# Performance work log

Measured on AMD Instinct MI355X. Metric: run time of the kernel, lower is better.

The kernel has to match this reference:

```python
import jax, jax.numpy as jnp
import numpy as np

SOS_TOKEN = 2
T = 1024      # sequence / max_length
H = 256       # embedding_dim == GRU hidden size
V = 50000     # vocab_size


def gru_cell(e, h, w_ih, w_hh, b_ih, b_hh):
    # PyTorch nn.GRU cell math. e, h: [H]; w_ih, w_hh: [3H, H]; b_*: [3H]
    gi = w_ih @ e + b_ih
    gh = w_hh @ h + b_hh
    i_r, i_z, i_n = jnp.split(gi, 3)
    h_r, h_z, h_n = jnp.split(gh, 3)
    r = jax.nn.sigmoid(i_r + h_r)
    z = jax.nn.sigmoid(i_z + h_z)
    n = jnp.tanh(i_n + r * h_n)
    return (1.0 - z) * n + z * h


def setup_inputs() -> dict:
    key = jax.random.key(0)
    ks = jax.random.split(key, 14)
    s = 1.0 / np.sqrt(H)
    def u(k, shape):
        return jax.random.uniform(k, shape, jnp.float32, -s, s)
    return {
        "x": jax.random.randint(ks[0], (T,), 0, V),
        "enc_emb": jax.random.normal(ks[1], (V, H), jnp.float32),
        "enc_w_ih": u(ks[2], (3 * H, H)),
        "enc_w_hh": u(ks[3], (3 * H, H)),
        "enc_b_ih": u(ks[4], (3 * H,)),
        "enc_b_hh": u(ks[5], (3 * H,)),
        "dec_emb": jax.random.normal(ks[6], (V, H), jnp.float32),
        "dec_w_ih": u(ks[7], (3 * H, H)),
        "dec_w_hh": u(ks[8], (3 * H, H)),
        "dec_b_ih": u(ks[9], (3 * H,)),
        "dec_b_hh": u(ks[10], (3 * H,)),
        "w_out": u(ks[11], (V, H)),
        "b_out": u(ks[12], (V,)),
    }


def reference(x, enc_emb, enc_w_ih, enc_w_hh, enc_b_ih, enc_b_hh,
              dec_emb, dec_w_ih, dec_w_hh, dec_b_ih, dec_b_hh, w_out, b_out):
    # ---- Encoder: embed whole sequence, scan GRU to final hidden ----
    emb_seq = enc_emb[x]                      # [T, H] (no relu in encoder)

    def enc_step(h, e):
        return gru_cell(e, h, enc_w_ih, enc_w_hh, enc_b_ih, enc_b_hh), None

    h_enc, _ = jax.lax.scan(enc_step, jnp.zeros((H,), emb_seq.dtype), emb_seq)

    # ---- Decoder: greedy argmax feedback, per-step log-softmax ----
    def dec_step(carry, _):
        h, tok = carry
        e = jax.nn.relu(dec_emb[tok])         # embed + relu
        h = gru_cell(e, h, dec_w_ih, dec_w_hh, dec_b_ih, dec_b_hh)
        logits = w_out @ h + b_out            # [V]
        logp = jax.nn.log_softmax(logits)
        tok = jnp.argmax(logp)                # topk(1) greedy feedback
        return (h, tok), logp

    init = (h_enc, jnp.asarray(SOS_TOKEN, x.dtype))
    _, decoder_outputs = jax.lax.scan(dec_step, init, None, length=T)
    return decoder_outputs                    # [T, V] log-probs
```

## Files before the change

### kernel.cpp

```cpp
#include <hip/hip_runtime.h>
#include <stdint.h>

#define TSEQ 1024
#define H 256
#define H3 768
#define NV 50000
#define NBLK 256
#define NTHR 512
#define RPB 196
#define SOS_TOK 2
#define SPIN_LIM (1 << 20)
#define NEB 4
#define EEL 64
#define EROWS 192

#define WS_SALT   0
#define WS_HENC   1024
#define WS_PMX    8192
#define WS_REC    16384
#define WS_GIENC  65536
#define WS_TABLE  (65536 + TSEQ * H3 * 4)
#define TABLE_BYTES ((size_t)NV * H3 * 4)

using u64 = unsigned long long;

__device__ __forceinline__ void awr(u64* p, u64 v) {
  __hip_atomic_store(p, v, __ATOMIC_RELAXED, __HIP_MEMORY_SCOPE_AGENT);
}
__device__ __forceinline__ u64 ard(u64* p) {
  return __hip_atomic_load(p, __ATOMIC_RELAXED, __HIP_MEMORY_SCOPE_AGENT);
}
__device__ __forceinline__ u64 pkf(unsigned tg, float f) {
  return ((u64)tg << 32) | (u64)__float_as_uint(f);
}
__device__ __forceinline__ float upf(u64 w) { return __uint_as_float((unsigned)w); }
__device__ __forceinline__ unsigned tagof(u64 w) { return (unsigned)(w >> 32); }

__device__ __forceinline__ void agpr_w(float& dst, float v) {
  asm volatile("v_accvgpr_write_b32 %0, %1" : "=a"(dst) : "v"(v));
}
__device__ __forceinline__ float agpr_r(float src) {
  float v;
  asm volatile("v_accvgpr_read_b32 %0, %1" : "=v"(v) : "a"(src));
  return v;
}

extern "C" __global__ void k_init(char* ws) {
  if (threadIdx.x == 0) {
    unsigned* s = (unsigned*)(ws + WS_SALT);
    *s = *s + 1u;
  }
}

extern "C" __global__ void k_enc_gi(const int* __restrict__ x, const float* __restrict__ emb,
                                    const float* __restrict__ wih, const float* __restrict__ bih,
                                    float* __restrict__ gi) {
  int tid = threadIdx.x;
  int t0 = blockIdx.x * 16;
  __shared__ float4 se4[16][H / 4];
  float* se = (float*)se4;
  for (int idx = tid; idx < 16 * H; idx += 256) {
    int j = idx >> 8, k = idx & 255;
    se[j * H + k] = emb[(size_t)x[t0 + j] * H + k];
  }
  __syncthreads();
  for (int q = 0; q < 3; q++) {
    int r = q * H + tid;
    const float4* w4 = (const float4*)(wih + (size_t)r * H);
    float bb = bih[r];
    float a[16];
#pragma unroll
    for (int j = 0; j < 16; j++) a[j] = bb;
    for (int k = 0; k < H / 4; k++) {
      float4 wv = w4[k];
#pragma unroll
      for (int j = 0; j < 16; j++) {
        float4 ev = se4[j][k];
        a[j] += wv.x * ev.x + wv.y * ev.y + wv.z * ev.z + wv.w * ev.w;
      }
    }
#pragma unroll
    for (int j = 0; j < 16; j++) gi[(size_t)(t0 + j) * H3 + r] = a[j];
  }
}

extern "C" __global__ void k_table(const float* __restrict__ emb, const float* __restrict__ wih,
                                   const float* __restrict__ bih, float* __restrict__ table) {
  int tid = threadIdx.x;
  int v0 = blockIdx.x * 16;
  __shared__ float4 se4[16][H / 4];
  float* se = (float*)se4;
  for (int idx = tid; idx < 16 * H; idx += 256) {
    int j = idx >> 8, k = idx & 255;
    se[j * H + k] = fmaxf(emb[(size_t)(v0 + j) * H + k], 0.f);
  }
  __syncthreads();
  for (int q = 0; q < 3; q++) {
    int r = q * H + tid;
    const float4* w4 = (const float4*)(wih + (size_t)r * H);
    float bb = bih[r];
    float a[16];
#pragma unroll
    for (int j = 0; j < 16; j++) a[j] = bb;
    for (int k = 0; k < H / 4; k++) {
      float4 wv = w4[k];
#pragma unroll
      for (int j = 0; j < 16; j++) {
        float4 ev = se4[j][k];
        a[j] += wv.x * ev.x + wv.y * ev.y + wv.z * ev.z + wv.w * ev.w;
      }
    }
#pragma unroll
    for (int j = 0; j < 16; j++) table[(size_t)(v0 + j) * H3 + r] = a[j];
  }
}

extern "C" __global__ void __launch_bounds__(NTHR, 1)
k_enc(const float* __restrict__ enc_whh, const float* __restrict__ enc_bhh,
      char* __restrict__ ws) {
  const int b = blockIdx.x, tid = threadIdx.x;
  u64* henc = (u64*)(ws + WS_HENC);
  const float* gi_enc = (const float*)(ws + WS_GIENC);
  __shared__ float sh_h[H];
  __shared__ float sh_ghE[EROWS];
  __shared__ int sh_abort;
  if (tid == 0) sh_abort = 0;

  const int p2 = tid >> 1, hf = tid & 1;
  const bool ract = (p2 < EROWS);
  const int q = p2 >> 6, ri = p2 & 63;
  const size_t grow = ract ? (size_t)(q * H + b * EEL + ri) : 0;
  float wa[128];
  {
    const float4* wp = (const float4*)(enc_whh + grow * H + hf * 128);
#pragma unroll
    for (int k = 0; k < 32; ++k) {
      float4 v = ract ? wp[k] : make_float4(0.f, 0.f, 0.f, 0.f);
      agpr_w(wa[4 * k + 0], v.x);
      agpr_w(wa[4 * k + 1], v.y);
      agpr_w(wa[4 * k + 2], v.z);
      agpr_w(wa[4 * k + 3], v.w);
    }
  }
  const int el = b * EEL + tid;
  float be0 = 0.f, be1 = 0.f, be2 = 0.f;
  if (tid < EEL) { be0 = enc_bhh[el]; be1 = enc_bhh[H + el]; be2 = enc_bhh[2 * H + el]; }
  const unsigned salt = *(volatile unsigned*)(ws + WS_SALT);
  const unsigned tb32 = salt * 65536u;
  __syncthreads();

  float hb = 0.f;
  if (tid < EEL) {
    float g0 = gi_enc[el], g1 = gi_enc[H + el], g2 = gi_enc[2 * H + el];
    float r = 1.f / (1.f + expf(-(g0 + be0)));
    float z = 1.f / (1.f + expf(-(g1 + be1)));
    float n = tanhf(g2 + r * be2);
    hb = (1.f - z) * n;
    awr(henc + 256 + el, pkf(tb32 + 1u, hb));
  }
  int ec = 1;
  for (int t = 1; t < TSEQ; ++t) {
    float g0 = 0.f, g1 = 0.f, g2 = 0.f;
    if (tid < EEL) {
      g0 = gi_enc[(size_t)t * H3 + el];
      g1 = gi_enc[(size_t)t * H3 + H + el];
      g2 = gi_enc[(size_t)t * H3 + 2 * H + el];
    }
    if (tid < H) {
      u64* pp_ = henc + (size_t)(ec & 1) * 256 + tid;
      u64 w = 0; int n_ = 0;
      do { w = ard(pp_); } while (tagof(w) != tb32 + (unsigned)ec && ++n_ < SPIN_LIM);
      if (tagof(w) != tb32 + (unsigned)ec) sh_abort = 1;
      sh_h[tid] = upf(w);
    }
    __syncthreads();
    if (sh_abort) return;
    float pcc = 0.f;
    if (ract) {
      const float4* h4 = ((const float4*)sh_h) + hf * 32;
#pragma unroll
      for (int k = 0; k < 32; ++k) {
        float4 hv = h4[k];
        pcc += agpr_r(wa[4 * k + 0]) * hv.x + agpr_r(wa[4 * k + 1]) * hv.y +
               agpr_r(wa[4 * k + 2]) * hv.z + agpr_r(wa[4 * k + 3]) * hv.w;
      }
    }
    pcc += __shfl_xor(pcc, 1);
    if (ract && hf == 0) sh_ghE[p2] = pcc;
    __syncthreads();
    ++ec;
    if (tid < EEL) {
      float r = 1.f / (1.f + expf(-(g0 + (sh_ghE[tid] + be0))));
      float z = 1.f / (1.f + expf(-(g1 + (sh_ghE[EEL + tid] + be1))));
      float n = tanhf(g2 + r * (sh_ghE[2 * EEL + tid] + be2));
      hb = (1.f - z) * n + z * hb;
      awr(henc + (size_t)(ec & 1) * 256 + el, pkf(tb32 + (unsigned)ec, hb));
    }
  }
}

extern "C" __global__ void __launch_bounds__(NTHR, 1)
k_dec(const float* __restrict__ dec_emb, const float* __restrict__ dec_wih,
      const float* __restrict__ dec_whh, const float* __restrict__ dec_bih,
      const float* __restrict__ dec_bhh, const float* __restrict__ w_out,
      const float* __restrict__ b_out, float* __restrict__ out,
      char* __restrict__ ws, int use_table) {
  const int b = blockIdx.x, tid = threadIdx.x;
  u64* henc = (u64*)(ws + WS_HENC);
  u64* pmx = (u64*)(ws + WS_PMX);
  u64* rec = (u64*)(ws + WS_REC);
  const float* table = (const float*)(ws + WS_TABLE);

  __shared__ float sh_h[H];
  __shared__ float sh_wd[3][H];
  __shared__ float sh_wi[3][H];
  __shared__ float sh_gi[H3];
  __shared__ float gh_lds[H3];
  __shared__ float sh_lg[2][RPB];
  __shared__ float sh_bout[RPB];
  __shared__ float sh_gh3[3];
  __shared__ float sh_rv[8];
  __shared__ float sh_mv[8];
  __shared__ int sh_mi[8];
  __shared__ float sh_sv[8];
  __shared__ float sh_mv2[8];
  __shared__ int sh_mi2[8];
  __shared__ float sh_sv2[8];
  __shared__ float sh_e[H];
  __shared__ int sh_abort;

  if (tid == 0) sh_abort = 0;

  for (int k = tid; k < 3 * H; k += NTHR) {
    int q = k >> 8, c = k & 255;
    sh_wd[q][c] = dec_whh[((size_t)(3 * b + q)) * H + c];
    if (!use_table) sh_wi[q][c] = dec_wih[((size_t)(3 * b + q)) * H + c];
  }
  const float bd0 = dec_bhh[3 * b], bd1 = dec_bhh[3 * b + 1], bd2 = dec_bhh[3 * b + 2];
  float bi0 = 0.f, bi1 = 0.f, bi2 = 0.f;
  if (!use_table) { bi0 = dec_bih[3 * b]; bi1 = dec_bih[3 * b + 1]; bi2 = dec_bih[3 * b + 2]; }
  const int rowbase = b * RPB;
  const int nrows = min(RPB, max(0, NV - rowbase));
  const int p = tid >> 1, hf = tid & 1;
  const bool wact = (p < nrows);
  float wa[128];
  {
    const float4* wp = (const float4*)(w_out + (size_t)(rowbase + (wact ? p : 0)) * H + hf * 128);
#pragma unroll
    for (int i = 0; i < 32; ++i) {
      float4 v = wact ? wp[i] : make_float4(0.f, 0.f, 0.f, 0.f);
      agpr_w(wa[4 * i + 0], v.x);
      agpr_w(wa[4 * i + 1], v.y);
      agpr_w(wa[4 * i + 2], v.z);
      agpr_w(wa[4 * i + 3], v.w);
    }
  }
  if (tid < RPB) sh_bout[tid] = (tid < nrows) ? b_out[rowbase + tid] : 0.f;
  const unsigned salt = *(volatile unsigned*)(ws + WS_SALT);
  const unsigned tb32 = salt * 65536u;
  const unsigned tb24 = salt * 4096u;
  __syncthreads();

  auto wave_maxidx = [&](float& mv, int& mi) {
#pragma unroll
    for (int off = 32; off >= 1; off >>= 1) {
      float ov = __shfl_xor(mv, off);
      int oi = __shfl_xor(mi, off);
      if (ov > mv || (ov == mv && oi < mi)) { mv = ov; mi = oi; }
    }
  };
  auto row3 = [&](const float(&wr)[3][H], float bb0, float bb1, float bb2, const float* vin) {
    int q = tid >> 7, i = tid & 127;
    float pp = 0.f;
    if (q < 3) pp = wr[q][2 * i] * vin[2 * i] + wr[q][2 * i + 1] * vin[2 * i + 1];
#pragma unroll
    for (int off = 32; off >= 1; off >>= 1) pp += __shfl_xor(pp, off);
    if (q < 3 && (tid & 63) == 0) sh_rv[tid >> 6] = pp;
    __syncthreads();
    if (tid == 0) {
      sh_gh3[0] = sh_rv[0] + sh_rv[1] + bb0;
      sh_gh3[1] = sh_rv[2] + sh_rv[3] + bb1;
      sh_gh3[2] = sh_rv[4] + sh_rv[5] + bb2;
    }
    __syncthreads();
  };
  auto gru_step = [&]() {
    if (tid < H) {
      float gir = sh_gi[tid], giz = sh_gi[H + tid], gin = sh_gi[2 * H + tid];
      float ghr = gh_lds[tid], ghz = gh_lds[H + tid], ghn = gh_lds[2 * H + tid];
      float r = 1.f / (1.f + expf(-(gir + ghr)));
      float z = 1.f / (1.f + expf(-(giz + ghz)));
      float n = tanhf(gin + r * ghn);
      sh_h[tid] = (1.f - z) * n + z * sh_h[tid];
    }
    __syncthreads();
  };
  auto spin_rec3 = [&](unsigned tg, float* dst) {
    if (tid < NBLK) {
      u64* pp_ = rec + (size_t)(tg & 1) * 1024 + (size_t)tid * 4;
      u64 w0 = 0, w1 = 0, w2 = 0; int n = 0; bool ok;
      do {
        w0 = ard(pp_ + 0); w1 = ard(pp_ + 1); w2 = ard(pp_ + 2);
        ok = (tagof(w0) == tg) & (tagof(w1) == tg) & (tagof(w2) == tg);
      } while (!ok && ++n < SPIN_LIM);
      if (!ok) sh_abort = 1;
      dst[3 * tid] = upf(w0); dst[3 * tid + 1] = upf(w1); dst[3 * tid + 2] = upf(w2);
    }
    __syncthreads();
  };

  if (tid < NBLK) {
    u64* pp_ = henc + tid;
    u64 w = 0; int n_ = 0;
    do { w = ard(pp_); } while (tagof(w) != tb32 + (unsigned)TSEQ && ++n_ < SPIN_LIM);
    if (tagof(w) != tb32 + (unsigned)TSEQ) sh_abort = 1;
    sh_h[tid] = upf(w);
  }
  __syncthreads();
  if (sh_abort) return;

  int e = TSEQ;
  row3(sh_wd, bd0, bd1, bd2, sh_h);
  ++e;
  {
    unsigned tg = tb32 + (unsigned)e;
    if (tid == 0) {
      u64* d = rec + (size_t)(tg & 1) * 1024 + (size_t)b * 4;
      awr(d + 0, pkf(tg, sh_gh3[0]));
      awr(d + 1, pkf(tg, sh_gh3[1]));
      awr(d + 2, pkf(tg, sh_gh3[2]));
    }
    spin_rec3(tg, gh_lds);
    if (sh_abort) return;
  }

  int tok = SOS_TOK;
  float2 gp = make_float2(0.f, 0.f);
  if (use_table) {
    if (tid < 384) gp = *(const float2*)(table + (size_t)SOS_TOK * H3 + 2 * tid);
  } else {
    for (int j = tid; j < H; j += NTHR) sh_e[j] = fmaxf(dec_emb[(size_t)SOS_TOK * H + j], 0.f);
    __syncthreads();
    row3(sh_wi, bi0, bi1, bi2, sh_e);
    ++e;
    unsigned tg = tb32 + (unsigned)e;
    if (tid == 0) {
      u64* d = rec + (size_t)(tg & 1) * 1024 + (size_t)b * 4;
      awr(d + 0, pkf(tg, sh_gh3[0]));
      awr(d + 1, pkf(tg, sh_gh3[1]));
      awr(d + 2, pkf(tg, sh_gh3[2]));
    }
    spin_rec3(tg, sh_gi);
    if (sh_abort) return;
  }

  float lse_pend = 0.f;
  for (int t = 0; t < TSEQ; ++t) {
    const int cur = t & 1;
    if (use_table) {
      if (tid < 384) { sh_gi[2 * tid] = gp.x; sh_gi[2 * tid + 1] = gp.y; }
    }
    __syncthreads();
    gru_step();
    float acc = 0.f;
    if (wact) {
      const float4* h4 = ((const float4*)sh_h) + hf * 32;
#pragma unroll
      for (int i = 0; i < 32; ++i) {
        float4 hv = h4[i];
        acc += agpr_r(wa[4 * i + 0]) * hv.x + agpr_r(wa[4 * i + 1]) * hv.y +
               agpr_r(wa[4 * i + 2]) * hv.z + agpr_r(wa[4 * i + 3]) * hv.w;
      }
    }
    acc += __shfl_xor(acc, 1);
    if (wact && hf == 0) sh_lg[cur][p] = acc + sh_bout[p];
    __syncthreads();
    ++e;
    const unsigned tg32 = tb32 + (unsigned)e;
    const unsigned tg24 = (tb24 + (unsigned)e) & 0xFFFFFFu;
    float mv = (tid < nrows) ? sh_lg[cur][tid] : -INFINITY;
    int mi = (tid < nrows) ? (rowbase + tid) : 0x7fffffff;
    wave_maxidx(mv, mi);
    if ((tid & 63) == 0) { sh_mv[tid >> 6] = mv; sh_mi[tid >> 6] = mi; }
    __syncthreads();
    float bmax = sh_mv[0]; int bidx = sh_mi[0];
#pragma unroll
    for (int k = 1; k < 8; ++k)
      if (sh_mv[k] > bmax || (sh_mv[k] == bmax && sh_mi[k] < bidx)) { bmax = sh_mv[k]; bidx = sh_mi[k]; }
    if (tid == 0) {
      u64 g = ((u64)tg24 << 40) | ((u64)__float_as_uint(bmax) << 8) |
              (u64)((unsigned)(bidx - rowbase) & 0xFFu);
      awr(pmx + (size_t)(e & 1) * 256 + b, g);
    }
    float ec = (tid < nrows) ? __expf(sh_lg[cur][tid] - bmax) : 0.f;
#pragma unroll
    for (int off = 32; off >= 1; off >>= 1) ec += __shfl_xor(ec, off);
    if ((tid & 63) == 0) sh_sv[tid >> 6] = ec;
    __syncthreads();
    float bsum = 0.f;
#pragma unroll
    for (int k = 0; k < 8; ++k) bsum += sh_sv[k];
    row3(sh_wd, bd0, bd1, bd2, sh_h);
    if (tid == 0) {
      u64* d = rec + (size_t)(e & 1) * 1024 + (size_t)b * 4;
      awr(d + 0, pkf(tg32, sh_gh3[0]));
      awr(d + 1, pkf(tg32, sh_gh3[1]));
      awr(d + 2, pkf(tg32, sh_gh3[2]));
      awr(d + 3, pkf(tg32, bsum));
    }
    if (t > 0 && tid < nrows)
      out[(size_t)(t - 1) * NV + rowbase + tid] = sh_lg[cur ^ 1][tid] - lse_pend;
    float bm_e = -INFINITY; int ie = 0x7fffffff;
    {
      u64 w = 0;
      if (tid < NBLK) {
        u64* pp_ = pmx + (size_t)(e & 1) * 256 + tid;
        int n = 0;
        do { w = ard(pp_); } while ((unsigned)(w >> 40) != tg24 && ++n < SPIN_LIM);
        if ((unsigned)(w >> 40) != tg24) sh_abort = 1;
        bm_e = __uint_as_float((unsigned)((w >> 8) & 0xFFFFFFFFu));
        ie = tid * RPB + (int)(w & 0xFFu);
      }
      __syncthreads();
      if (sh_abort) return;
    }
    float mv2 = bm_e; int mi2 = ie;
    wave_maxidx(mv2, mi2);
    if ((tid & 63) == 0) { sh_mv2[tid >> 6] = mv2; sh_mi2[tid >> 6] = mi2; }
    __syncthreads();
    float gmax = sh_mv2[0]; int gidx = sh_mi2[0];
#pragma unroll
    for (int k = 1; k < 8; ++k)
      if (sh_mv2[k] > gmax || (sh_mv2[k] == gmax && sh_mi2[k] < gidx)) { gmax = sh_mv2[k]; gidx = sh_mi2[k]; }
    tok = gidx;
    if (use_table && t + 1 < TSEQ) {
      if (tid < 384) gp = *(const float2*)(table + (size_t)tok * H3 + 2 * tid);
    }
    float sv = 0.f;
    if (tid < NBLK) {
      u64* pp_ = rec + (size_t)(e & 1) * 1024 + (size_t)tid * 4;
      u64 w0 = 0, w1 = 0, w2 = 0, w3 = 0; int n = 0; bool ok;
      do {
        w0 = ard(pp_ + 0); w1 = ard(pp_ + 1); w2 = ard(pp_ + 2); w3 = ard(pp_ + 3);
        ok = (tagof(w0) == tg32) & (tagof(w1) == tg32) & (tagof(w2) == tg32) &
             (tagof(w3) == tg32);
      } while (!ok && ++n < SPIN_LIM);
      if (!ok) sh_abort = 1;
      gh_lds[3 * tid] = upf(w0); gh_lds[3 * tid + 1] = upf(w1); gh_lds[3 * tid + 2] = upf(w2);
      sv = upf(w3);
    }
    __syncthreads();
    if (sh_abort) return;
    float c = (tid < NBLK) ? sv * __expf(bm_e - gmax) : 0.f;
#pragma unroll
    for (int off = 32; off >= 1; off >>= 1) c += __shfl_xor(c, off);
    if ((tid & 63) == 0) sh_sv2[tid >> 6] = c;
    __syncthreads();
    float S = 0.f;
#pragma unroll
    for (int k = 0; k < 8; ++k) S += sh_sv2[k];
    lse_pend = gmax + logf(S);
    if (!use_table && t + 1 < TSEQ) {
      for (int j = tid; j < H; j += NTHR) sh_e[j] = fmaxf(dec_emb[(size_t)tok * H + j], 0.f);
      __syncthreads();
      row3(sh_wi, bi0, bi1, bi2, sh_e);
      ++e;
      unsigned tgg = tb32 + (unsigned)e;
      if (tid == 0) {
        u64* d = rec + (size_t)(tgg & 1) * 1024 + (size_t)b * 4;
        awr(d + 0, pkf(tgg, sh_gh3[0]));
        awr(d + 1, pkf(tgg, sh_gh3[1]));
        awr(d + 2, pkf(tgg, sh_gh3[2]));
      }
      spin_rec3(tgg, sh_gi);
      if (sh_abort) return;
    }
  }
  if (tid < nrows)
    out[(size_t)(TSEQ - 1) * NV + rowbase + tid] = sh_lg[(TSEQ - 1) & 1][tid] - lse_pend;
}

extern "C" void kernel_launch(void* const* d_in, const int* in_sizes, int n_in,
                              void* d_out, int out_size, void* d_ws, size_t ws_size,
                              hipStream_t stream) {
  (void)in_sizes; (void)n_in; (void)out_size;
  const int* x = (const int*)d_in[0];
  const float* enc_emb = (const float*)d_in[1];
  const float* enc_wih = (const float*)d_in[2];
  const float* enc_whh = (const float*)d_in[3];
  const float* enc_bih = (const float*)d_in[4];
  const float* enc_bhh = (const float*)d_in[5];
  const float* dec_emb = (const float*)d_in[6];
  const float* dec_wih = (const float*)d_in[7];
  const float* dec_whh = (const float*)d_in[8];
  const float* dec_bih = (const float*)d_in[9];
  const float* dec_bhh = (const float*)d_in[10];
  const float* w_out = (const float*)d_in[11];
  const float* b_out = (const float*)d_in[12];
  float* out = (float*)d_out;
  char* ws = (char*)d_ws;

  int use_table = (ws_size >= (size_t)WS_TABLE + TABLE_BYTES) ? 1 : 0;

  k_init<<<1, 64, 0, stream>>>(ws);
  k_enc_gi<<<TSEQ / 16, 256, 0, stream>>>(x, enc_emb, enc_wih, enc_bih, (float*)(ws + WS_GIENC));
  if (use_table)
    k_table<<<NV / 16, 256, 0, stream>>>(dec_emb, dec_wih, dec_bih, (float*)(ws + WS_TABLE));
  k_enc<<<NEB, NTHR, 0, stream>>>(enc_whh, enc_bhh, ws);
  k_dec<<<NBLK, NTHR, 0, stream>>>(dec_emb, dec_wih, dec_whh, dec_bih, dec_bhh,
                                   w_out, b_out, out, ws, use_table);
}
```

Baseline: 9.354 ms.

## Overlap decoder table build with encoder scan and colocate encoder blocks on one XCD

The separate table kernel is folded into the encoder launch. 64 blocks start, and four of them, chosen through an XCD-ID roster so they share one XCD, run the serial encoder GRU. The rest pull table tiles from a dynamic atomic counter, so the table precompute overlaps the latency-bound encoder scan. When all four workers are on the same XCD and a probe handshake succeeds, they exchange hidden state through workgroup-scope stores and L2 atomic reads instead of agent-scope traffic, with a fallback to the old path otherwise. The decoder also defers the log-sum-exp reduction by one step, so it runs after the partial-sum publish rather than in the critical exchange path. This adds spin-based roster and verdict handshakes, and relies on the XCD placement and L2-coherence assumptions holding.

Measured after the change: 8.644 ms. -7.6%, faster.

```diff
diff --git a/kernel.cpp b/kernel.cpp
--- a/kernel.cpp
+++ b/kernel.cpp
@@ -10,14 +10,19 @@
 #define RPB 196
 #define SOS_TOK 2
 #define SPIN_LIM (1 << 20)
-#define NEB 4
+#define NEB_L 64
+#define NEW 4
 #define EEL 64
 #define EROWS 192
 
 #define WS_SALT   0
+#define WS_DISP   64
+#define WS_ROSTER 128
+#define WS_VERD   832
 #define WS_HENC   1024
 #define WS_PMX    8192
 #define WS_REC    16384
+#define WS_EHL2   32768
 #define WS_GIENC  65536
 #define WS_TABLE  (65536 + TSEQ * H3 * 4)
 #define TABLE_BYTES ((size_t)NV * H3 * 4)
@@ -30,11 +35,27 @@
 __device__ __forceinline__ u64 ard(u64* p) {
   return __hip_atomic_load(p, __ATOMIC_RELAXED, __HIP_MEMORY_SCOPE_AGENT);
 }
+__device__ __forceinline__ unsigned ard32(unsigned* p) {
+  return __hip_atomic_load(p, __ATOMIC_RELAXED, __HIP_MEMORY_SCOPE_AGENT);
+}
 __device__ __forceinline__ u64 pkf(unsigned tg, float f) {
   return ((u64)tg << 32) | (u64)__float_as_uint(f);
 }
+__device__ __forceinline__ u64 pku(unsigned tg, unsigned v) {
+  return ((u64)tg << 32) | (u64)v;
+}
 __device__ __forceinline__ float upf(u64 w) { return __uint_as_float((unsigned)w); }
 __device__ __forceinline__ unsigned tagof(u64 w) { return (unsigned)(w >> 32); }
+
+__device__ __forceinline__ void wgst(u64* p, u64 v) {
+  __hip_atomic_store(p, v, __ATOMIC_RELAXED, __HIP_MEMORY_SCOPE_WORKGROUP);
+}
+__device__ __forceinline__ u64 wgld(u64* p) {
+  u64 v;
+  asm volatile("global_atomic_add_x2 %0, %1, %2, off sc0\n\ts_waitcnt vmcnt(0)"
+               : "=v"(v) : "v"(p), "v"(0ull) : "memory");
+  return v;
+}
 
 __device__ __forceinline__ void agpr_w(float& dst, float v) {
   asm volatile("v_accvgpr_write_b32 %0, %1" : "=a"(dst) : "v"(v));
@@ -49,6 +70,8 @@
   if (threadIdx.x == 0) {
     unsigned* s = (unsigned*)(ws + WS_SALT);
     *s = *s + 1u;
+    *(unsigned*)(ws + WS_DISP) = 0u;
+    for (int i = 0; i < 8; ++i) *(unsigned*)(ws + WS_ROSTER + i * 64) = 0u;
   }
 }
 
@@ -84,52 +107,124 @@
   }
 }
 
-extern "C" __global__ void k_table(const float* __restrict__ emb, const float* __restrict__ wih,
-                                   const float* __restrict__ bih, float* __restrict__ table) {
-  int tid = threadIdx.x;
-  int v0 = blockIdx.x * 16;
-  __shared__ float4 se4[16][H / 4];
-  float* se = (float*)se4;
-  for (int idx = tid; idx < 16 * H; idx += 256) {
-    int j = idx >> 8, k = idx & 255;
-    se[j * H + k] = fmaxf(emb[(size_t)(v0 + j) * H + k], 0.f);
-  }
-  __syncthreads();
-  for (int q = 0; q < 3; q++) {
-    int r = q * H + tid;
-    const float4* w4 = (const float4*)(wih + (size_t)r * H);
-    float bb = bih[r];
-    float a[16];
-#pragma unroll
-    for (int j = 0; j < 16; j++) a[j] = bb;
-    for (int k = 0; k < H / 4; k++) {
-      float4 wv = w4[k];
-#pragma unroll
-      for (int j = 0; j < 16; j++) {
-        float4 ev = se4[j][k];
-        a[j] += wv.x * ev.x + wv.y * ev.y + wv.z * ev.z + wv.w * ev.w;
-      }
-    }
-#pragma unroll
-    for (int j = 0; j < 16; j++) table[(size_t)(v0 + j) * H3 + r] = a[j];
-  }
-}
-
 extern "C" __global__ void __launch_bounds__(NTHR, 1)
 k_enc(const float* __restrict__ enc_whh, const float* __restrict__ enc_bhh,
-      char* __restrict__ ws) {
+      const float* __restrict__ dec_emb, const float* __restrict__ dec_wih,
+      const float* __restrict__ dec_bih, char* __restrict__ ws, int use_table) {
   const int b = blockIdx.x, tid = threadIdx.x;
   u64* henc = (u64*)(ws + WS_HENC);
+  u64* ehl2 = (u64*)(ws + WS_EHL2);
+  u64* verd = (u64*)(ws + WS_VERD);
   const float* gi_enc = (const float*)(ws + WS_GIENC);
+  float* table = (float*)(ws + WS_TABLE);
+
+  __shared__ float se[16 * H];
   __shared__ float sh_h[H];
   __shared__ float sh_ghE[EROWS];
-  __shared__ int sh_abort;
+  __shared__ int sh_xcd, sh_rank, sh_chosen, sh_u, sh_abort;
   if (tid == 0) sh_abort = 0;
+
+  const unsigned salt = *(volatile unsigned*)(ws + WS_SALT);
+  const unsigned tb32 = salt * 65536u;
+
+  if (tid == 0) {
+    unsigned x;
+    asm volatile("s_getreg_b32 %0, hwreg(HW_REG_XCC_ID)" : "=s"(x));
+    int myxcd = (int)(x & 7u);
+    unsigned* rost = (unsigned*)(ws + WS_ROSTER);
+    int rank = (int)__hip_atomic_fetch_add(rost + myxcd * 16, 1u,
+                                           __ATOMIC_RELAXED, __HIP_MEMORY_SCOPE_AGENT);
+    long n_ = 0;
+    unsigned tot = 0;
+    do {
+      tot = 0;
+      for (int i = 0; i < 8; ++i) tot += ard32(rost + i * 16);
+      if (++n_ > 2000000L) break;
+      __builtin_amdgcn_s_sleep(1);
+    } while (tot < (unsigned)NEB_L);
+    int chosen = -1;
+    for (int i = 0; i < 8; ++i) {
+      unsigned c = ard32(rost + i * 16);
+      if (chosen < 0 && c >= (unsigned)NEW) chosen = i;
+    }
+    sh_xcd = myxcd; sh_rank = rank; sh_chosen = chosen;
+  }
+  __syncthreads();
+  bool isw;
+  int role;
+  if (sh_chosen >= 0) { isw = (sh_xcd == sh_chosen) && (sh_rank < NEW); role = sh_rank; }
+  else { isw = (b < NEW); role = b; }
+
+  if (!isw) {
+    if (!use_table) return;
+    unsigned* disp = (unsigned*)(ws + WS_DISP);
+    for (;;) {
+      if (tid == 0)
+        sh_u = (int)__hip_atomic_fetch_add(disp, 1u, __ATOMIC_RELAXED,
+                                           __HIP_MEMORY_SCOPE_AGENT);
+      __syncthreads();
+      int u = sh_u;
+      if (u >= NV / 16) return;
+      int v0 = u * 16;
+      for (int idx = tid; idx < 16 * H; idx += NTHR) {
+        int j = idx >> 8, k2 = idx & 255;
+        se[j * H + k2] = fmaxf(dec_emb[(size_t)(v0 + j) * H + k2], 0.f);
+      }
+      __syncthreads();
+      for (int r = tid; r < H3; r += NTHR) {
+        const float4* w4 = (const float4*)(dec_wih + (size_t)r * H);
+        float bb = dec_bih[r];
+        float a[16];
+#pragma unroll
+        for (int j = 0; j < 16; j++) a[j] = bb;
+        for (int k = 0; k < H / 4; k++) {
+          float4 wv = w4[k];
+#pragma unroll
+          for (int j = 0; j < 16; j++) {
+            const float4 ev = ((const float4*)se)[j * (H / 4) + k];
+            a[j] += wv.x * ev.x + wv.y * ev.y + wv.z * ev.z + wv.w * ev.w;
+          }
+        }
+#pragma unroll
+        for (int j = 0; j < 16; j++)
+          table[(size_t)(v0 + j) * H3 + r] = a[j];
+      }
+      __syncthreads();
+    }
+  }
+
+  const int el = role * EEL + (tid & 63);
+  const int elw = role * EEL + tid;
+
+  int okl = 1;
+  for (int k = 0; k < 8 && okl; ++k) {
+    unsigned wtg = tb32 + 50001u + (unsigned)k;
+    if (tid < EEL) wgst(ehl2 + (size_t)(k & 1) * 256 + elw, pku(wtg, 0u));
+    int lim = (k == 0) ? 6000 : 2000;
+    int myok = 1;
+    if (tid < H) {
+      u64* pp_ = ehl2 + (size_t)(k & 1) * 256 + tid;
+      u64 w = 0; int n_ = 0;
+      do { w = wgld(pp_); } while (tagof(w) != wtg && ++n_ < lim);
+      myok = (tagof(w) == wtg);
+    }
+    okl = __syncthreads_and(myok);
+  }
+  const unsigned tagV = tb32 + 60001u;
+  if (tid == 0) awr(verd + role, pku(tagV, okl ? 0u : 1u));
+  int fb = 0;
+  if (tid < NEW) {
+    u64 w = 0; int n_ = 0;
+    do { w = ard(verd + tid); } while (tagof(w) != tagV && ++n_ < SPIN_LIM);
+    fb = (tagof(w) != tagV) ? 1 : (int)(w & 1u);
+  }
+  const bool l2m = __syncthreads_and(fb == 0);
+  u64* EX = l2m ? ehl2 : henc;
 
   const int p2 = tid >> 1, hf = tid & 1;
   const bool ract = (p2 < EROWS);
   const int q = p2 >> 6, ri = p2 & 63;
-  const size_t grow = ract ? (size_t)(q * H + b * EEL + ri) : 0;
+  const size_t grow = ract ? (size_t)(q * H + role * EEL + ri) : 0;
   float wa[128];
   {
     const float4* wp = (const float4*)(enc_whh + grow * H + hf * 128);
@@ -142,11 +237,8 @@
       agpr_w(wa[4 * k + 3], v.w);
     }
   }
-  const int el = b * EEL + tid;
   float be0 = 0.f, be1 = 0.f, be2 = 0.f;
   if (tid < EEL) { be0 = enc_bhh[el]; be1 = enc_bhh[H + el]; be2 = enc_bhh[2 * H + el]; }
-  const unsigned salt = *(volatile unsigned*)(ws + WS_SALT);
-  const unsigned tb32 = salt * 65536u;
   __syncthreads();
 
   float hb = 0.f;
@@ -156,7 +248,8 @@
     float z = 1.f / (1.f + expf(-(g1 + be1)));
     float n = tanhf(g2 + r * be2);
     hb = (1.f - z) * n;
-    awr(henc + 256 + el, pkf(tb32 + 1u, hb));
+    u64 w = pkf(tb32 + 1u, hb);
+    if (l2m) wgst(EX + 256 + elw, w); else awr(EX + 256 + elw, w);
   }
   int ec = 1;
   for (int t = 1; t < TSEQ; ++t) {
@@ -167,9 +260,10 @@
       g2 = gi_enc[(size_t)t * H3 + 2 * H + el];
     }
     if (tid < H) {
-      u64* pp_ = henc + (size_t)(ec & 1) * 256 + tid;
+      u64* pp_ = EX + (size_t)(ec & 1) * 256 + tid;
       u64 w = 0; int n_ = 0;
-      do { w = ard(pp_); } while (tagof(w) != tb32 + (unsigned)ec && ++n_ < SPIN_LIM);
+      if (l2m) { do { w = wgld(pp_); } while (tagof(w) != tb32 + (unsigned)ec && ++n_ < SPIN_LIM); }
+      else     { do { w = ard(pp_); }  while (tagof(w) != tb32 + (unsigned)ec && ++n_ < SPIN_LIM); }
       if (tagof(w) != tb32 + (unsigned)ec) sh_abort = 1;
       sh_h[tid] = upf(w);
     }
@@ -194,9 +288,12 @@
       float z = 1.f / (1.f + expf(-(g1 + (sh_ghE[EEL + tid] + be1))));
       float n = tanhf(g2 + r * (sh_ghE[2 * EEL + tid] + be2));
       hb = (1.f - z) * n + z * hb;
-      awr(henc + (size_t)(ec & 1) * 256 + el, pkf(tb32 + (unsigned)ec, hb));
-    }
-  }
+      u64 w = pkf(tb32 + (unsigned)ec, hb);
+      u64* d = EX + (size_t)(ec & 1) * 256 + elw;
+      if (l2m) wgst(d, w); else awr(d, w);
+    }
+  }
+  if (l2m && tid < EEL) awr(henc + elw, pkf(tb32 + (unsigned)TSEQ, hb));
 }
 
 extern "C" __global__ void __launch_bounds__(NTHR, 1)
@@ -354,7 +451,7 @@
     if (sh_abort) return;
   }
 
-  float lse_pend = 0.f;
+  float sv_p = 0.f, bm_p = -INFINITY, gm_p = 0.f;
   for (int t = 0; t < TSEQ; ++t) {
     const int cur = t & 1;
     if (use_table) {
@@ -392,24 +489,36 @@
               (u64)((unsigned)(bidx - rowbase) & 0xFFu);
       awr(pmx + (size_t)(e & 1) * 256 + b, g);
     }
-    float ec = (tid < nrows) ? __expf(sh_lg[cur][tid] - bmax) : 0.f;
-#pragma unroll
-    for (int off = 32; off >= 1; off >>= 1) ec += __shfl_xor(ec, off);
-    if ((tid & 63) == 0) sh_sv[tid >> 6] = ec;
-    __syncthreads();
-    float bsum = 0.f;
-#pragma unroll
-    for (int k = 0; k < 8; ++k) bsum += sh_sv[k];
     row3(sh_wd, bd0, bd1, bd2, sh_h);
     if (tid == 0) {
       u64* d = rec + (size_t)(e & 1) * 1024 + (size_t)b * 4;
       awr(d + 0, pkf(tg32, sh_gh3[0]));
       awr(d + 1, pkf(tg32, sh_gh3[1]));
       awr(d + 2, pkf(tg32, sh_gh3[2]));
-      awr(d + 3, pkf(tg32, bsum));
-    }
-    if (t > 0 && tid < nrows)
-      out[(size_t)(t - 1) * NV + rowbase + tid] = sh_lg[cur ^ 1][tid] - lse_pend;
+    }
+    float ec = (tid < nrows) ? __expf(sh_lg[cur][tid] - bmax) : 0.f;
+#pragma unroll
+    for (int off = 32; off >= 1; off >>= 1) ec += __shfl_xor(ec, off);
+    if ((tid & 63) == 0) sh_sv[tid >> 6] = ec;
+    __syncthreads();
+    float bsum = 0.f;
+#pragma unroll
+    for (int k = 0; k < 8; ++k) bsum += sh_sv[k];
+    if (tid == 0)
+      awr(rec + (size_t)(e & 1) * 1024 + (size_t)b * 4 + 3, pkf(tg32, bsum));
+    if (t > 0) {
+      float c = (tid < NBLK) ? sv_p * __expf(bm_p - gm_p) : 0.f;
+#pragma unroll
+      for (int off = 32; off >= 1; off >>= 1) c += __shfl_xor(c, off);
+      if ((tid & 63) == 0) sh_sv2[tid >> 6] = c;
+      __syncthreads();
+      float S = 0.f;
+#pragma unroll
+      for (int k = 0; k < 8; ++k) S += sh_sv2[k];
+      float lse = gm_p + logf(S);
+      if (tid < nrows)
+        out[(size_t)(t - 1) * NV + rowbase + tid] = sh_lg[cur ^ 1][tid] - lse;
+    }
     float bm_e = -INFINITY; int ie = 0x7fffffff;
     {
       u64 w = 0;
@@ -451,15 +560,7 @@
     }
     __syncthreads();
     if (sh_abort) return;
-    float c = (tid < NBLK) ? sv * __expf(bm_e - gmax) : 0.f;
-#pragma unroll
-    for (int off = 32; off >= 1; off >>= 1) c += __shfl_xor(c, off);
-    if ((tid & 63) == 0) sh_sv2[tid >> 6] = c;
-    __syncthreads();
-    float S = 0.f;
-#pragma unroll
-    for (int k = 0; k < 8; ++k) S += sh_sv2[k];
-    lse_pend = gmax + logf(S);
+    sv_p = sv; bm_p = bm_e; gm_p = gmax;
     if (!use_table && t + 1 < TSEQ) {
       for (int j = tid; j < H; j += NTHR) sh_e[j] = fmaxf(dec_emb[(size_t)tok * H + j], 0.f);
       __syncthreads();
@@ -476,8 +577,19 @@
       if (sh_abort) return;
     }
   }
-  if (tid < nrows)
-    out[(size_t)(TSEQ - 1) * NV + rowbase + tid] = sh_lg[(TSEQ - 1) & 1][tid] - lse_pend;
+  {
+    float c = (tid < NBLK) ? sv_p * __expf(bm_p - gm_p) : 0.f;
+#pragma unroll
+    for (int off = 32; off >= 1; off >>= 1) c += __shfl_xor(c, off);
+    if ((tid & 63) == 0) sh_sv2[tid >> 6] = c;
+    __syncthreads();
+    float S = 0.f;
+#pragma unroll
+    for (int k = 0; k < 8; ++k) S += sh_sv2[k];
+    float lse = gm_p + logf(S);
+    if (tid < nrows)
+      out[(size_t)(TSEQ - 1) * NV + rowbase + tid] = sh_lg[(TSEQ - 1) & 1][tid] - lse;
+  }
 }
 
 extern "C" void kernel_launch(void* const* d_in, const int* in_sizes, int n_in,
@@ -504,9 +616,7 @@
 
   k_init<<<1, 64, 0, stream>>>(ws);
   k_enc_gi<<<TSEQ / 16, 256, 0, stream>>>(x, enc_emb, enc_wih, enc_bih, (float*)(ws + WS_GIENC));
-  if (use_table)
-    k_table<<<NV / 16, 256, 0, stream>>>(dec_emb, dec_wih, dec_bih, (float*)(ws + WS_TABLE));
-  k_enc<<<NEB, NTHR, 0, stream>>>(enc_whh, enc_bhh, ws);
+  k_enc<<<NEB_L, NTHR, 0, stream>>>(enc_whh, enc_bhh, dec_emb, dec_wih, dec_bih, ws, use_table);
   k_dec<<<NBLK, NTHR, 0, stream>>>(dec_emb, dec_wih, dec_whh, dec_bih, dec_bhh,
                                    w_out, b_out, out, ws, use_table);
 }
```
